# Optimization experiments

Measured on AMD Instinct MI355X. Metric: run time of the kernel, lower is better.

## Reference

```python
import jax, jax.numpy as jnp
import numpy as np

DIM = 192
HEADS = 6
B = 4
H = 64
W = 64
L = H * W  # kv length must equal h*w for the torch 'else' repeat branch
TOPK = 4
N_EXPERTS = 12
PADS = [0, 1, 2] * 4
GROUPS = [1] * 6 + [DIM] * 6


def conv2d(x, w, b=None, pad=0, groups=1):
    out = jax.lax.conv_general_dilated(
        x, w, (1, 1), [(pad, pad), (pad, pad)],
        dimension_numbers=("NCHW", "OIHW", "NCHW"),
        feature_group_count=groups)
    if b is not None:
        out = out + b[None, :, None, None]
    return out


def l2norm(x):
    # torch F.normalize(dim=-1): x / max(||x||_2, 1e-12)
    return x / jnp.maximum(jnp.linalg.norm(x, axis=-1, keepdims=True), 1e-12)


def attention_ca(I, T, proj_w):
    b, c, h, w = I.shape
    l = T.shape[2]
    # F.avg_pool1d(kv.transpose(1,2), 4) pools the CHANNEL dim, kernel=stride=4
    pooled = T.transpose(0, 2, 1).reshape(b, l, c // 4, 4).mean(-1)  # [b, l, c/4]
    x_pool = pooled.transpose(0, 2, 1)  # [b, c/4, l]
    q = l2norm(I.reshape(b, HEADS, c // HEADS, h * w))
    k = l2norm(x_pool.reshape(b, HEADS, c // (4 * HEADS), l))
    v = k  # v = normalize(x_pool) = k
    # h == 64 -> torch 'else' branch: repeat(1, 1, 4, 1) on channel dim
    k = jnp.tile(k, (1, 1, 4, 1))
    v = jnp.tile(v, (1, 1, 4, 1))
    attn = jax.nn.softmax(jnp.einsum("bhcl,bhdl->bhcd", q, k), axis=-1)
    out = jnp.einsum("bhcd,bhdl->bhcl", attn, v).reshape(b, c, h, w)
    return conv2d(out, proj_w)


def ex_forward(x, fmap, ex_ws, ex_bs, out_w, out_b):
    # AdaptiveAvgPool3d((1,1,12)) applied to a 4D tensor [b,c,h,w]:
    # full mean over dims 1 (c) and 2 (h), adaptive 12-bin pooling over dim 3 (w)
    m = fmap.mean(axis=(1, 2))  # [b, w]
    win = m.shape[-1]
    bins = [m[:, (i * win) // 12: -(-((i + 1) * win) // 12)].mean(-1) for i in range(12)]
    wvec = jax.nn.softmax(jnp.stack(bins, axis=-1), axis=-1)  # [b, 12]
    _, idx = jax.lax.top_k(wvec[0], TOPK)  # module uses batch element 0 only
    branches = [
        (lambda xx, j=j: conv2d(xx, ex_ws[j], ex_bs[j], pad=PADS[j], groups=GROUPS[j]))
        for j in range(N_EXPERTS)
    ]
    outs = [jax.lax.switch(idx[i], branches, x) for i in range(TOPK)]
    return conv2d(jnp.concatenate(outs, axis=1), out_w, out_b, pad=1)


def forward(I, T, temperature, ca1_proj_w, ex_ws, ex_bs, ex_out_w, ex_out_b,
            kv_w, kv_dw_w, q_dw_w, proj_w):
    b, c, h, w = I.shape
    fmap = attention_ca(I, T, ca1_proj_w)
    fmap = ex_forward(I, fmap, ex_ws, ex_bs, ex_out_w, ex_out_b)
    kv = conv2d(conv2d(fmap, kv_w), kv_dw_w, pad=1, groups=2 * c)
    k, v = jnp.split(kv, 2, axis=1)
    q = conv2d(fmap, q_dw_w, pad=1, groups=c)
    q = l2norm(q.reshape(b, HEADS, c // HEADS, h * w))
    k = l2norm(k.reshape(b, HEADS, c // HEADS, h * w))
    v = v.reshape(b, HEADS, c // HEADS, h * w)
    attn = jax.nn.softmax(jnp.einsum("bhcl,bhdl->bhcd", q, k) * temperature[None], axis=-1)
    out = jnp.einsum("bhcd,bhdl->bhcl", attn, v).reshape(b, c, h, w)
    return conv2d(out, proj_w)


def setup_inputs() -> dict:
    key = jax.random.key(0)
    ks = jax.random.split(key, 64)
    def rn(i, shape, s=0.05):
        return jax.random.normal(ks[i], shape, dtype=jnp.float32) * s
    d = DIM
    inp = {
        "I": rn(0, (B, d, H, W), 1.0),
        "T": rn(1, (B, d, L), 1.0),
        "temperature": jnp.ones((HEADS, 1, 1), dtype=jnp.float32),
        "ca1_proj_w": rn(2, (d, d, 1, 1)),
        "ex_out_w": rn(3, (d, 4 * d, 3, 3), 0.02),
        "ex_out_b": rn(4, (d,), 0.01),
        "kv_w": rn(5, (2 * d, d, 1, 1)),
        "kv_dw_w": rn(6, (2 * d, 1, 3, 3)),
        "q_dw_w": rn(7, (d, 1, 3, 3)),
        "proj_w": rn(8, (d, d, 1, 1)),
    }
    ksz = [1, 3, 5] * 4
    for j in range(N_EXPERTS):
        cin = d if j < 6 else 1
        inp[f"ex_w{j}"] = rn(10 + j, (d, cin, ksz[j], ksz[j]), 0.05)
        inp[f"ex_b{j}"] = rn(30 + j, (d,), 0.01)
    return inp


def reference(I, T, temperature, ca1_proj_w,
              ex_w0, ex_w1, ex_w2, ex_w3, ex_w4, ex_w5,
              ex_w6, ex_w7, ex_w8, ex_w9, ex_w10, ex_w11,
              ex_b0, ex_b1, ex_b2, ex_b3, ex_b4, ex_b5,
              ex_b6, ex_b7, ex_b8, ex_b9, ex_b10, ex_b11,
              ex_out_w, ex_out_b, kv_w, kv_dw_w, q_dw_w, proj_w):
    ex_ws = [ex_w0, ex_w1, ex_w2, ex_w3, ex_w4, ex_w5,
             ex_w6, ex_w7, ex_w8, ex_w9, ex_w10, ex_w11]
    ex_bs = [ex_b0, ex_b1, ex_b2, ex_b3, ex_b4, ex_b5,
             ex_b6, ex_b7, ex_b8, ex_b9, ex_b10, ex_b11]
    return forward(I, T, temperature, ca1_proj_w, ex_ws, ex_bs,
                   ex_out_w, ex_out_b, kv_w, kv_dw_w, q_dw_w, proj_w)
```

## Files before the change

kernel.cpp:

```cpp
#include <hip/hip_runtime.h>
#include <math.h>


struct ExPtrs { const float* w[12]; const float* b[12]; };
struct BfPtrs { const short* adt[6]; const float* bias[6]; };

typedef __attribute__((ext_vector_type(8))) short short8v;
typedef __attribute__((ext_vector_type(4))) short short4v;
typedef __attribute__((ext_vector_type(16))) float f32x16;

__device__ __forceinline__ void fma4(float4& a, float s, const float4& v) {
    a.x = fmaf(s, v.x, a.x); a.y = fmaf(s, v.y, a.y);
    a.z = fmaf(s, v.z, a.z); a.w = fmaf(s, v.w, a.w);
}

__device__ __forceinline__ short f2bf(float v) {
    unsigned u = __float_as_uint(v);
    return (short)((u + 0x7FFFu + ((u >> 16) & 1u)) >> 16);
}

__device__ __forceinline__ float bf2f(short v) {
    return __uint_as_float(((unsigned)(unsigned short)v) << 16);
}

__global__ void zero_kernel(float* __restrict__ p, int n) {
    for (int i = blockIdx.x * 256 + threadIdx.x; i < n; i += gridDim.x * 256) p[i] = 0.f;
}

__global__ void packIbf_kernel(const float* __restrict__ I, short* __restrict__ Ibf) {
    const int n = 4 * 68 * 68 * 192;
    for (int o = blockIdx.x * 256 + threadIdx.x; o < n; o += gridDim.x * 256) {
        int ch = o % 192;
        int t = o / 192;
        int xx = t % 68; t /= 68;
        int yy = t % 68;
        int b = t / 68;
        short v = 0;
        if (yy >= 2 && yy < 66 && xx >= 2 && xx < 66)
            v = f2bf(I[(((size_t)(b * 192 + ch)) << 12) + (yy - 2) * 64 + (xx - 2)]);
        Ibf[o] = v;
    }
}

__global__ void packAd_kernel(const float* __restrict__ w, short* __restrict__ Ad, int K2) {
    int n = K2 * 6 * 12 * 64 * 8;
    for (int o = blockIdx.x * 256 + threadIdx.x; o < n; o += gridDim.x * 256) {
        int j = o & 7;
        int t = o >> 3;
        int l = t & 63; t >>= 6;
        int ks = t % 12; t /= 12;
        int mt = t % 6;
        int tap = t / 6;
        int oc = mt * 32 + (l & 31);
        int ic = ks * 16 + (l >> 5) * 8 + j;
        Ad[o] = f2bf(w[(((size_t)oc * 192) + ic) * K2 + tap]);
    }
}

__global__ void packA_kernel(const float* __restrict__ exow, short* __restrict__ At) {
    const int n = 9 * 6 * 48 * 64 * 8;
    for (int o = blockIdx.x * 256 + threadIdx.x; o < n; o += gridDim.x * 256) {
        int j = o & 7;
        int t = o >> 3;
        int l = t & 63; t >>= 6;
        int ks = t % 48; t /= 48;
        int mt = t % 6;
        int tap = t / 6;
        int oc = mt * 32 + (l & 31);
        int icg = ks * 16 + (l >> 5) * 8 + j;
        At[o] = f2bf(exow[((size_t)oc * 768 + icg) * 9 + tap]);
    }
}

__global__ void wtr8_kernel(const float* __restrict__ w, float* __restrict__ wt,
                            int OCg, int IC, int K2) {
    int n = OCg * IC * K2 * 8;
    for (int o = blockIdx.x * 256 + threadIdx.x; o < n; o += gridDim.x * 256) {
        int u = o & 7;
        int t = o >> 3;
        int kk = t % K2;
        int t2 = t / K2;
        int ic = t2 % IC;
        int og = t2 / IC;
        wt[o] = w[(((size_t)(og * 8 + u)) * IC + ic) * K2 + kk];
    }
}

__global__ void packWdw_kernel(ExPtrs ep, float* __restrict__ wdwt) {
    int o = blockIdx.x * 256 + threadIdx.x;
    if (o >= 6 * 25 * 192) return;
    int ch = o % 192;
    int t = o / 192;
    int kk = t % 25;
    int e = t / 25;
    int j = e + 6;
    int K = 1 + 2 * (j % 3);
    int K2 = K * K;
    wdwt[o] = (kk < K2) ? ep.w[j][(size_t)ch * K2 + kk] : 0.f;
}


__global__ void pool64_kernel(const float* __restrict__ T, double* __restrict__ xp) {
    int j = blockIdx.x;
    for (int l = threadIdx.x; l < 4096; l += 256) {
        const float* t = T + ((size_t)(4 * j)) * 4096 + l;
        double s = (double)t[0] + (double)t[4096] + (double)t[2 * 4096] + (double)t[3 * 4096];
        xp[(size_t)j * 4096 + l] = 0.25 * s;
    }
}

__global__ void norm64_f32_kernel(const float* __restrict__ src, double* __restrict__ dst) {
    size_t off = (size_t)blockIdx.x * 4096;
    double acc = 0.0;
    for (int i = threadIdx.x; i < 4096; i += 256) { double v = src[off + i]; acc += v * v; }
    __shared__ double red[256];
    red[threadIdx.x] = acc; __syncthreads();
    for (int st = 128; st > 0; st >>= 1) {
        if (threadIdx.x < st) red[threadIdx.x] += red[threadIdx.x + st];
        __syncthreads();
    }
    double scale = 1.0 / fmax(sqrt(red[0]), 1e-12);
    for (int i = threadIdx.x; i < 4096; i += 256) dst[off + i] = src[off + i] * scale;
}

__global__ void norm64_f64_kernel(double* __restrict__ buf) {
    size_t off = (size_t)blockIdx.x * 4096;
    double acc = 0.0;
    for (int i = threadIdx.x; i < 4096; i += 256) { double v = buf[off + i]; acc += v * v; }
    __shared__ double red[256];
    red[threadIdx.x] = acc; __syncthreads();
    for (int st = 128; st > 0; st >>= 1) {
        if (threadIdx.x < st) red[threadIdx.x] += red[threadIdx.x + st];
        __syncthreads();
    }
    double scale = 1.0 / fmax(sqrt(red[0]), 1e-12);
    for (int i = threadIdx.x; i < 4096; i += 256) buf[off + i] *= scale;
}

__global__ void attnA64p_kernel(const double* __restrict__ qn, const double* __restrict__ kn,
                                double* __restrict__ PA) {
    int hh = blockIdx.x, cc = blockIdx.y;
    int t = threadIdx.x;
    int c = t >> 3, d = t & 7;
    const double* q = qn + ((size_t)(hh * 32 + c)) * 4096 + cc * 256;
    const double* k = kn + ((size_t)(hh * 8 + d)) * 4096 + cc * 256;
    double acc = 0.0;
    for (int i = 0; i < 256; ++i) acc += q[i] * k[i];
    PA[((size_t)((hh * 32 + c) * 8 + d)) * 16 + cc] = acc;
}

__global__ void attnA64r_kernel(const double* __restrict__ PA, double* __restrict__ A) {
    int hh = blockIdx.x;
    int t = threadIdx.x;
    int c = t >> 3, d = t & 7;
    double acc = 0.0;
    const double* p = PA + ((size_t)((hh * 32 + c) * 8 + d)) * 16;
    for (int cc = 0; cc < 16; ++cc) acc += p[cc];
    __shared__ double S[32][8];
    S[c][d] = acc;
    __syncthreads();
    if (t < 32) {
        double mx = -1e300;
        for (int j = 0; j < 8; ++j) mx = fmax(mx, S[t][j]);
        double e[8], sum = 0.0;
        for (int j = 0; j < 8; ++j) { e[j] = exp(S[t][j] - mx); sum += e[j]; }
        double inv = 1.0 / sum;
        for (int j = 0; j < 8; ++j) A[((size_t)(hh * 32 + t)) * 8 + j] = e[j] * inv;
    }
}

__global__ void kcol64_kernel(const double* __restrict__ kn, double* __restrict__ kcol) {
    int j = blockIdx.x, x = threadIdx.x;
    const double* s = kn + (size_t)j * 4096 + x;
    double acc = 0.0;
    for (int y = 0; y < 64; ++y) acc += s[y * 64];
    kcol[j * 64 + x] = acc;
}

__global__ void wsum64_kernel(const float* __restrict__ ca1, double* __restrict__ wsum) {
    int ic = threadIdx.x;
    if (ic >= 192) return;
    double acc = 0.0;
    for (int oc = 0; oc < 192; ++oc) acc += (double)ca1[(size_t)oc * 192 + ic];
    wsum[ic] = acc;
}

__global__ void mroute64_kernel(const double* __restrict__ A, const double* __restrict__ kcol,
                                const double* __restrict__ wsum, double* __restrict__ m) {
    int x = threadIdx.x;
    if (x >= 64) return;
    double acc = 0.0;
    for (int ic = 0; ic < 192; ++ic) {
        int hh = ic >> 5;
        double s = 0.0;
        #pragma unroll
        for (int d = 0; d < 8; ++d)
            s += A[(size_t)ic * 8 + d] * kcol[(hh * 8 + d) * 64 + x];
        acc += wsum[ic] * s;
    }
    m[x] = acc / (192.0 * 64.0);
}

__global__ void route64_kernel(const double* __restrict__ m, int* __restrict__ idx) {
    if (threadIdx.x != 0) return;
    double bins[12];
    for (int i = 0; i < 12; ++i) {
        int st = (i * 64) / 12;
        int en = ((i + 1) * 64 + 11) / 12;
        double s = 0.0;
        for (int j = st; j < en; ++j) s += m[j];
        bins[i] = s / (double)(en - st);
    }
    bool used[12] = {};
    for (int s = 0; s < 4; ++s) {
        int best = 0; double bv = -1e300;
        for (int j = 0; j < 12; ++j)
            if (!used[j] && bins[j] > bv) { best = j; bv = bins[j]; }
        used[best] = true;
        idx[s] = best;
    }
}


__global__ void rownorm_kernel(const float* __restrict__ src, float* __restrict__ dst) {
    size_t off = (size_t)blockIdx.x * 4096;
    const float* s = src + off;
    float acc = 0.f;
    for (int i = threadIdx.x; i < 4096; i += 256) { float v = s[i]; acc += v * v; }
    __shared__ float red[256];
    red[threadIdx.x] = acc; __syncthreads();
    for (int st = 128; st > 0; st >>= 1) {
        if (threadIdx.x < st) red[threadIdx.x] += red[threadIdx.x + st];
        __syncthreads();
    }
    float scale = 1.0f / fmaxf(sqrtf(red[0]), 1e-12f);
    float* d = dst + off;
    for (int i = threadIdx.x; i < 4096; i += 256) d[i] = s[i] * scale;
}

template<int KK>
__device__ __forceinline__ void dmf_body(const short* __restrict__ Ad,
                                         const short* __restrict__ Ibf,
                                         const float* __restrict__ bias,
                                         short* __restrict__ Ebf, int cslot,
                                         int b, int y, short* __restrict__ sb) {
    constexpr int P = (KK - 1) / 2;
    int tid = threadIdx.x;
    int lane = tid & 63, wave = tid >> 6;
    int u = blockIdx.y * 4 + wave;
    int mt = u >> 1, nt = u & 1;
    int c32 = lane & 31, hi = lane >> 5;
    f32x16 acc;
    #pragma unroll
    for (int r = 0; r < 16; ++r)
        acc[r] = bias[mt * 32 + (r & 3) + 8 * (r >> 2) + 4 * hi];
    for (int rr = 0; rr < KK; ++rr) {
        const short* src = Ibf + ((size_t)(b * 68 + y + 2 - P + rr)) * 68 * 192;
        if (rr > 0) __syncthreads();
        for (int g2 = tid; g2 < 68 * 24; g2 += 256) {
            int px = g2 / 24, ck = g2 % 24;
            *(short8v*)(sb + px * 200 + ck * 8) = *(const short8v*)(src + px * 192 + ck * 8);
        }
        __syncthreads();
        for (int dx = 0; dx < KK; ++dx) {
            int tap = rr * KK + dx;
            const short* Ab = Ad + (((size_t)(tap * 6 + mt)) * 12) * 512 + (size_t)lane * 8;
            const short* Bb = sb + ((2 - P) + dx + nt * 32 + c32) * 200 + hi * 8;
            #pragma unroll 4
            for (int ks = 0; ks < 12; ++ks) {
                short8v av = *(const short8v*)(Ab + ks * 512);
                short8v bv = *(const short8v*)(Bb + ks * 16);
                acc = __builtin_amdgcn_mfma_f32_32x32x16_bf16(av, bv, acc, 0, 0, 0);
            }
        }
    }
    int xo = nt * 32 + c32;
    short* dbase = Ebf + (((size_t)(b * 66 + y + 1)) * 68 + (xo + 1)) * 384
                   + cslot * 192 + mt * 32 + 4 * hi;
    #pragma unroll
    for (int g = 0; g < 4; ++g) {
        short4v o;
        #pragma unroll
        for (int r = 0; r < 4; ++r) o[r] = f2bf(acc[g * 4 + r]);
        *(short4v*)(dbase + g * 8) = o;
    }
}

__global__ void dense_mfma_kernel(BfPtrs bp, const short* __restrict__ Ibf,
                                  const int* __restrict__ idx, int slot,
                                  short* __restrict__ Ebf, int cslot) {
    __shared__ short sb[68 * 200];
    int j = idx[slot];
    j = j < 0 ? 0 : (j > 11 ? 11 : j);
    if (j >= 6) return;
    int y = blockIdx.x, b = blockIdx.z;
    int m = j % 3;
    if (m == 0) dmf_body<1>(bp.adt[j], Ibf, bp.bias[j], Ebf, cslot, b, y, sb);
    else if (m == 1) dmf_body<3>(bp.adt[j], Ibf, bp.bias[j], Ebf, cslot, b, y, sb);
    else dmf_body<5>(bp.adt[j], Ibf, bp.bias[j], Ebf, cslot, b, y, sb);
}

template<int KK>
__device__ __forceinline__ void dw_body(const short* __restrict__ Ibf,
                                        const float* __restrict__ wt,
                                        float bias,
                                        short* __restrict__ Ebf, int cslot,
                                        int b, int pg, int ch) {
    constexpr int P = (KK - 1) / 2;
    constexpr int K2 = KK * KK;
    float wreg[K2];
    #pragma unroll
    for (int kk = 0; kk < K2; ++kk) wreg[kk] = wt[kk * 192 + ch];
    #pragma unroll
    for (int u = 0; u < 4; ++u) {
        int px = pg * 4 + u;
        int y = px >> 6, x = px & 63;
        const short* base = Ibf + ((size_t)(b * 68 + y + 2 - P)) * 68 * 192
                            + (size_t)(x + 2 - P) * 192 + ch;
        float acc = bias;
        #pragma unroll
        for (int ky = 0; ky < KK; ++ky)
            #pragma unroll
            for (int kx = 0; kx < KK; ++kx)
                acc = fmaf(wreg[ky * KK + kx], bf2f(base[(ky * 68 + kx) * 192]), acc);
        Ebf[(((size_t)(b * 66 + y + 1)) * 68 + (x + 1)) * 384 + cslot * 192 + ch] = f2bf(acc);
    }
}

__global__ void dw_bf_kernel(const short* __restrict__ Ibf, const float* __restrict__ wdwt,
                             ExPtrs ep, const int* __restrict__ idx, int slot,
                             short* __restrict__ Ebf, int cslot) {
    int j = idx[slot];
    j = j < 0 ? 0 : (j > 11 ? 11 : j);
    if (j < 6) return;
    int ch = threadIdx.x;
    int pg = blockIdx.x, b = blockIdx.y;
    const float* wt = wdwt + (size_t)(j - 6) * 25 * 192;
    float bias = ep.b[j][ch];
    int m = j % 3;
    if (m == 0) dw_body<1>(Ibf, wt, bias, Ebf, cslot, b, pg, ch);
    else if (m == 1) dw_body<3>(Ibf, wt, bias, Ebf, cslot, b, pg, ch);
    else dw_body<5>(Ibf, wt, bias, Ebf, cslot, b, pg, ch);
}

__global__ void exout_mfma_kernel(const short* __restrict__ At, const short* __restrict__ Ebf,
                                  const float* __restrict__ bias, float* __restrict__ out,
                                  int pass) {
    __shared__ short sb[68 * 392];
    int y = blockIdx.x, b = blockIdx.z;
    int tid = threadIdx.x;
    int lane = tid & 63, wave = tid >> 6;
    int u = blockIdx.y * 4 + wave;
    int mt = u >> 1, nt = u & 1;
    int c32 = lane & 31, hi = lane >> 5;
    float* dst = out + ((size_t)(b * 192 + mt * 32)) * 4096 + y * 64 + nt * 32 + c32;
    f32x16 acc;
    if (pass == 0) {
        #pragma unroll
        for (int r = 0; r < 16; ++r)
            acc[r] = bias[mt * 32 + (r & 3) + 8 * (r >> 2) + 4 * hi];
    } else {
        #pragma unroll
        for (int r = 0; r < 16; ++r)
            acc[r] = dst[(size_t)((r & 3) + 8 * (r >> 2) + 4 * hi) * 4096];
    }
    for (int rr = 0; rr < 3; ++rr) {
        const short* src = Ebf + ((size_t)(b * 66 + y + rr)) * 68 * 384;
        if (rr > 0) __syncthreads();
        for (int g2 = tid; g2 < 68 * 48; g2 += 256) {
            int px = g2 / 48, ck = g2 % 48;
            *(short8v*)(sb + px * 392 + ck * 8) = *(const short8v*)(src + px * 384 + ck * 8);
        }
        __syncthreads();
        for (int dx = 0; dx < 3; ++dx) {
            int tap = rr * 3 + dx;
            const short* Ab = At + (((size_t)(tap * 6 + mt)) * 48 + pass * 24) * 512
                              + (size_t)lane * 8;
            const short* Bb = sb + (dx + nt * 32 + c32) * 392 + hi * 8;
            #pragma unroll 4
            for (int ks = 0; ks < 24; ++ks) {
                short8v av = *(const short8v*)(Ab + (size_t)ks * 512);
                short8v bv = *(const short8v*)(Bb + ks * 16);
                acc = __builtin_amdgcn_mfma_f32_32x32x16_bf16(av, bv, acc, 0, 0, 0);
            }
        }
    }
    #pragma unroll
    for (int r = 0; r < 16; ++r)
        dst[(size_t)((r & 3) + 8 * (r >> 2) + 4 * hi) * 4096] = acc[r];
}

__global__ void conv1x1_sw_kernel(const float* __restrict__ in, const float* __restrict__ wtg,
                                  float* __restrict__ out) {
    int tid = threadIdx.x;
    int xq = tid & 15, ry = tid >> 4;
    int tile = blockIdx.x, og = blockIdx.y, b = blockIdx.z;
    int p0 = tile * 1024 + ry * 64 + xq * 4;
    float4 acc[8] = {};
    const float* src = in + (size_t)b * 192 * 4096 + p0;
    const float* wp = wtg + (size_t)og * 192 * 8;
    for (int ic = 0; ic < 192; ic += 2) {
        float4 xv0 = *(const float4*)(src + (size_t)ic * 4096);
        float4 xv1 = *(const float4*)(src + (size_t)(ic + 1) * 4096);
        float4 wA0 = *(const float4*)(wp + ic * 8);
        float4 wB0 = *(const float4*)(wp + ic * 8 + 4);
        float4 wA1 = *(const float4*)(wp + ic * 8 + 8);
        float4 wB1 = *(const float4*)(wp + ic * 8 + 12);
        fma4(acc[0], wA0.x, xv0); fma4(acc[1], wA0.y, xv0);
        fma4(acc[2], wA0.z, xv0); fma4(acc[3], wA0.w, xv0);
        fma4(acc[4], wB0.x, xv0); fma4(acc[5], wB0.y, xv0);
        fma4(acc[6], wB0.z, xv0); fma4(acc[7], wB0.w, xv0);
        fma4(acc[0], wA1.x, xv1); fma4(acc[1], wA1.y, xv1);
        fma4(acc[2], wA1.z, xv1); fma4(acc[3], wA1.w, xv1);
        fma4(acc[4], wB1.x, xv1); fma4(acc[5], wB1.y, xv1);
        fma4(acc[6], wB1.z, xv1); fma4(acc[7], wB1.w, xv1);
    }
    float* dst = out + ((size_t)(b * 192 + og * 8)) * 4096 + p0;
    #pragma unroll
    for (int u = 0; u < 8; ++u)
        *(float4*)(dst + (size_t)u * 4096) = acc[u];
}

__global__ void dwconv_kernel(const float* __restrict__ in, const float* __restrict__ w,
                              float* __restrict__ out) {
    int l = blockIdx.x * 256 + threadIdx.x;
    int ch = blockIdx.y, b = blockIdx.z;
    int y = l >> 6, x = l & 63;
    const float* src = in + ((size_t)(b * 192 + ch)) * 4096;
    const float* wk = w + ch * 9;
    float acc = 0.f;
    #pragma unroll
    for (int ky = 0; ky < 3; ++ky)
        #pragma unroll
        for (int kx = 0; kx < 3; ++kx) {
            int yy = y + ky - 1, xx = x + kx - 1;
            if (yy >= 0 && yy < 64 && xx >= 0 && xx < 64)
                acc += wk[ky * 3 + kx] * src[yy * 64 + xx];
        }
    out[((size_t)(b * 192 + ch)) * 4096 + l] = acc;
}

__global__ void attnF_row_kernel(const float* __restrict__ qn, const float* __restrict__ kn,
                                 const float* __restrict__ temp, float* __restrict__ AF) {
    int row = blockIdx.x;
    int hh = (row >> 5) % 6, b = row / 192;
    int tid = threadIdx.x;
    const float* q = qn + ((size_t)(b * 192) + (row % 192)) * 4096;
    const float* kb = kn + ((size_t)(b * 192 + hh * 32)) * 4096;
    float acc[32];
    #pragma unroll
    for (int d = 0; d < 32; ++d) acc[d] = 0.f;
    for (int i = tid; i < 4096; i += 256) {
        float qv = q[i];
        #pragma unroll
        for (int d = 0; d < 32; ++d) acc[d] += qv * kb[(size_t)d * 4096 + i];
    }
    #pragma unroll
    for (int d = 0; d < 32; ++d) {
        acc[d] += __shfl_xor(acc[d], 32);
        acc[d] += __shfl_xor(acc[d], 16);
        acc[d] += __shfl_xor(acc[d], 8);
        acc[d] += __shfl_xor(acc[d], 4);
        acc[d] += __shfl_xor(acc[d], 2);
        acc[d] += __shfl_xor(acc[d], 1);
    }
    __shared__ float red[4][32];
    int wid = tid >> 6, lane = tid & 63;
    if (lane == 0) {
        #pragma unroll
        for (int d = 0; d < 32; ++d) red[wid][d] = acc[d];
    }
    __syncthreads();
    if (tid < 32) {
        float s = red[0][tid] + red[1][tid] + red[2][tid] + red[3][tid];
        s *= temp[hh];
        float mx = s;
        mx = fmaxf(mx, __shfl_xor(mx, 16));
        mx = fmaxf(mx, __shfl_xor(mx, 8));
        mx = fmaxf(mx, __shfl_xor(mx, 4));
        mx = fmaxf(mx, __shfl_xor(mx, 2));
        mx = fmaxf(mx, __shfl_xor(mx, 1));
        float e = expf(s - mx);
        float sum = e;
        sum += __shfl_xor(sum, 16);
        sum += __shfl_xor(sum, 8);
        sum += __shfl_xor(sum, 4);
        sum += __shfl_xor(sum, 2);
        sum += __shfl_xor(sum, 1);
        AF[(size_t)row * 32 + tid] = e / sum;
    }
}

__global__ void attnF_out_kernel(const float* __restrict__ AF, const float* __restrict__ v,
                                 float* __restrict__ out) {
    int l = blockIdx.x * 256 + threadIdx.x;
    int ch = blockIdx.y, b = blockIdx.z;
    int hh = ch >> 5, c = ch & 31;
    const float* a = AF + ((size_t)((b * 6 + hh) * 32 + c)) * 32;
    const float* vp = v + ((size_t)(b * 192 + hh * 32)) * 4096 + l;
    float acc = 0.f;
    #pragma unroll
    for (int d = 0; d < 32; ++d) acc += a[d] * vp[(size_t)d * 4096];
    out[((size_t)(b * 192 + ch)) * 4096 + l] = acc;
}

extern "C" void kernel_launch(void* const* d_in, const int* in_sizes, int n_in,
                              void* d_out, int out_size, void* d_ws, size_t ws_size,
                              hipStream_t stream) {
    const float* I    = (const float*)d_in[0];
    const float* T    = (const float*)d_in[1];
    const float* temp = (const float*)d_in[2];
    const float* ca1  = (const float*)d_in[3];
    const float* exow = (const float*)d_in[4];
    const float* exob = (const float*)d_in[5];
    const float* kvw  = (const float*)d_in[6];
    const float* kvdw = (const float*)d_in[7];
    const float* qdw  = (const float*)d_in[8];
    const float* projw= (const float*)d_in[9];
    ExPtrs ep;
    for (int j = 0; j < 12; ++j) {
        ep.w[j] = (const float*)d_in[10 + 2 * j];
        ep.b[j] = (const float*)d_in[11 + 2 * j];
    }

    float* ws   = (float*)d_ws;
    float* AF   = ws;
    int*   idxb = (int*)(ws + 24576);
    float* R0   = ws + 32768;
    float* R1   = R0 + 3145728;
    float* IbfF = R1 + 3145728;
    float* EbfF = IbfF + 3551232;
    double* dsm = (double*)(EbfF + 3446784);
    double* A64 = dsm;
    double* m64 = dsm + 1536;
    double* PA  = dsm + 1600;
    double* kcol = dsm + 26176;
    double* wsum = dsm + 29248;
    float* wtkv   = (float*)(dsm + 29440);
    float* wtproj = wtkv + 73728;
    float* wdwt   = wtproj + 36864;
    short* At     = (short*)(wdwt + 28800);
    short* Adt    = At + 1327104;
    size_t adtoff[6] = {0, 36864, 368640, 1290240, 1327104, 1658880};
    double* xpool64 = (double*)R0;
    double* qn64    = (double*)(R0 + 393216);
    short* Ibf = (short*)IbfF;
    short* Ebf = (short*)EbfF;
    float* KN = IbfF;
    float* V  = EbfF;
    BfPtrs bp;
    for (int j = 0; j < 6; ++j) { bp.adt[j] = Adt + adtoff[j]; bp.bias[j] = ep.b[j]; }
    float* out  = (float*)d_out;

    dim3 g(16, 192, 4), gs8(4, 24, 4), gmf(64, 3, 4), gdw(1024, 4);

    for (int j = 0; j < 6; ++j) {
        int KK = 1 + 2 * (j % 3);
        packAd_kernel<<<512, 256, 0, stream>>>(ep.w[j], Adt + adtoff[j], KK * KK);
    }
    packA_kernel<<<1024, 256, 0, stream>>>(exow, At);
    wtr8_kernel<<<256, 256, 0, stream>>>(kvw, wtkv, 48, 192, 1);
    wtr8_kernel<<<256, 256, 0, stream>>>(projw, wtproj, 24, 192, 1);
    packWdw_kernel<<<113, 256, 0, stream>>>(ep, wdwt);
    packIbf_kernel<<<2048, 256, 0, stream>>>(I, Ibf);

    pool64_kernel<<<48, 256, 0, stream>>>(T, xpool64);
    norm64_f32_kernel<<<192, 256, 0, stream>>>(I, qn64);
    norm64_f64_kernel<<<48, 256, 0, stream>>>(xpool64);
    attnA64p_kernel<<<dim3(6, 16), 256, 0, stream>>>(qn64, xpool64, PA);
    attnA64r_kernel<<<6, 256, 0, stream>>>(PA, A64);
    kcol64_kernel<<<48, 64, 0, stream>>>(xpool64, kcol);
    wsum64_kernel<<<1, 192, 0, stream>>>(ca1, wsum);
    mroute64_kernel<<<1, 64, 0, stream>>>(A64, kcol, wsum, m64);
    route64_kernel<<<1, 64, 0, stream>>>(m64, idxb);

    zero_kernel<<<2048, 256, 0, stream>>>(EbfF, 3446784);
    for (int s = 0; s < 4; ++s) {
        dense_mfma_kernel<<<gmf, 256, 0, stream>>>(bp, Ibf, idxb, s, Ebf, s & 1);
        dw_bf_kernel<<<gdw, 192, 0, stream>>>(Ibf, wdwt, ep, idxb, s, Ebf, s & 1);
        if (s == 1)
            exout_mfma_kernel<<<gmf, 256, 0, stream>>>(At, Ebf, exob, R1, 0);
        if (s == 3)
            exout_mfma_kernel<<<gmf, 256, 0, stream>>>(At, Ebf, exob, R1, 1);
    }

    conv1x1_sw_kernel<<<gs8, 256, 0, stream>>>(R1, wtkv, R0);
    dwconv_kernel<<<g, 256, 0, stream>>>(R0, kvdw, KN);
    rownorm_kernel<<<768, 256, 0, stream>>>(KN, KN);
    dwconv_kernel<<<g, 256, 0, stream>>>(R1, qdw, R0);
    rownorm_kernel<<<768, 256, 0, stream>>>(R0, R0);
    attnF_row_kernel<<<768, 256, 0, stream>>>(R0, KN, temp, AF);
    conv1x1_sw_kernel<<<gs8, 256, 0, stream>>>(R1, wtkv + 36864, R0);
    dwconv_kernel<<<g, 256, 0, stream>>>(R0, kvdw + 192 * 9, V);

    attnF_out_kernel<<<g, 256, 0, stream>>>(AF, V, R0);
    conv1x1_sw_kernel<<<gs8, 256, 0, stream>>>(R0, wtproj, out);
}
```

Baseline: 573.6 us.

## Give each MFMA wave both column tiles and split K into even/odd accumulators

In the dense expert conv and the output 3x3 conv MFMA kernels, each wave now computes one 32-row M tile across both 32-wide N tiles. Each A fragment is therefore loaded once and reused for two MFMAs. The K loop is split into even and odd accumulator chains that are summed at the end, which breaks the serial MFMA dependency. Blocks shrink to 3 waves (192 threads) and the grid y drops to 2. This raises register use (four 16-float accumulators per wave) and lowers the wave count per block, which may cut occupancy.

```diff
diff --git a/kernel.cpp b/kernel.cpp
--- a/kernel.cpp
+++ b/kernel.cpp
@@ -247,17 +247,18 @@
     constexpr int P = (KK - 1) / 2;
     int tid = threadIdx.x;
     int lane = tid & 63, wave = tid >> 6;
-    int u = blockIdx.y * 4 + wave;
-    int mt = u >> 1, nt = u & 1;
+    int mt = blockIdx.y * 3 + wave;
     int c32 = lane & 31, hi = lane >> 5;
-    f32x16 acc;
-    #pragma unroll
-    for (int r = 0; r < 16; ++r)
-        acc[r] = bias[mt * 32 + (r & 3) + 8 * (r >> 2) + 4 * hi];
+    f32x16 a0e, a0o, a1e, a1o;
+    #pragma unroll
+    for (int r = 0; r < 16; ++r) {
+        float bv_ = bias[mt * 32 + (r & 3) + 8 * (r >> 2) + 4 * hi];
+        a0e[r] = bv_; a1e[r] = bv_; a0o[r] = 0.f; a1o[r] = 0.f;
+    }
     for (int rr = 0; rr < KK; ++rr) {
         const short* src = Ibf + ((size_t)(b * 68 + y + 2 - P + rr)) * 68 * 192;
         if (rr > 0) __syncthreads();
-        for (int g2 = tid; g2 < 68 * 24; g2 += 256) {
+        for (int g2 = tid; g2 < 68 * 24; g2 += 192) {
             int px = g2 / 24, ck = g2 % 24;
             *(short8v*)(sb + px * 200 + ck * 8) = *(const short8v*)(src + px * 192 + ck * 8);
         }
@@ -265,24 +266,37 @@
         for (int dx = 0; dx < KK; ++dx) {
             int tap = rr * KK + dx;
             const short* Ab = Ad + (((size_t)(tap * 6 + mt)) * 12) * 512 + (size_t)lane * 8;
-            const short* Bb = sb + ((2 - P) + dx + nt * 32 + c32) * 200 + hi * 8;
-            #pragma unroll 4
-            for (int ks = 0; ks < 12; ++ks) {
-                short8v av = *(const short8v*)(Ab + ks * 512);
-                short8v bv = *(const short8v*)(Bb + ks * 16);
-                acc = __builtin_amdgcn_mfma_f32_32x32x16_bf16(av, bv, acc, 0, 0, 0);
+            const short* Bb0 = sb + ((2 - P) + dx + c32) * 200 + hi * 8;
+            const short* Bb1 = Bb0 + 32 * 200;
+            #pragma unroll 2
+            for (int k2 = 0; k2 < 6; ++k2) {
+                short8v ave = *(const short8v*)(Ab + (2 * k2) * 512);
+                short8v avo = *(const short8v*)(Ab + (2 * k2 + 1) * 512);
+                short8v b0e = *(const short8v*)(Bb0 + (2 * k2) * 16);
+                short8v b0o = *(const short8v*)(Bb0 + (2 * k2 + 1) * 16);
+                short8v b1e = *(const short8v*)(Bb1 + (2 * k2) * 16);
+                short8v b1o = *(const short8v*)(Bb1 + (2 * k2 + 1) * 16);
+                a0e = __builtin_amdgcn_mfma_f32_32x32x16_bf16(ave, b0e, a0e, 0, 0, 0);
+                a1e = __builtin_amdgcn_mfma_f32_32x32x16_bf16(ave, b1e, a1e, 0, 0, 0);
+                a0o = __builtin_amdgcn_mfma_f32_32x32x16_bf16(avo, b0o, a0o, 0, 0, 0);
+                a1o = __builtin_amdgcn_mfma_f32_32x32x16_bf16(avo, b1o, a1o, 0, 0, 0);
             }
         }
     }
-    int xo = nt * 32 + c32;
-    short* dbase = Ebf + (((size_t)(b * 66 + y + 1)) * 68 + (xo + 1)) * 384
-                   + cslot * 192 + mt * 32 + 4 * hi;
+    short* db0 = Ebf + (((size_t)(b * 66 + y + 1)) * 68 + (c32 + 1)) * 384
+                 + cslot * 192 + mt * 32 + 4 * hi;
+    short* db1 = Ebf + (((size_t)(b * 66 + y + 1)) * 68 + (32 + c32 + 1)) * 384
+                 + cslot * 192 + mt * 32 + 4 * hi;
     #pragma unroll
     for (int g = 0; g < 4; ++g) {
-        short4v o;
-        #pragma unroll
-        for (int r = 0; r < 4; ++r) o[r] = f2bf(acc[g * 4 + r]);
-        *(short4v*)(dbase + g * 8) = o;
+        short4v o0, o1;
+        #pragma unroll
+        for (int r = 0; r < 4; ++r) {
+            o0[r] = f2bf(a0e[g * 4 + r] + a0o[g * 4 + r]);
+            o1[r] = f2bf(a1e[g * 4 + r] + a1o[g * 4 + r]);
+        }
+        *(short4v*)(db0 + g * 8) = o0;
+        *(short4v*)(db1 + g * 8) = o1;
     }
 }
 
@@ -350,24 +364,29 @@
     int y = blockIdx.x, b = blockIdx.z;
     int tid = threadIdx.x;
     int lane = tid & 63, wave = tid >> 6;
-    int u = blockIdx.y * 4 + wave;
-    int mt = u >> 1, nt = u & 1;
+    int mt = blockIdx.y * 3 + wave;
     int c32 = lane & 31, hi = lane >> 5;
-    float* dst = out + ((size_t)(b * 192 + mt * 32)) * 4096 + y * 64 + nt * 32 + c32;
-    f32x16 acc;
+    float* d0 = out + ((size_t)(b * 192 + mt * 32)) * 4096 + y * 64 + c32;
+    float* d1 = d0 + 32;
+    f32x16 a0e, a0o, a1e, a1o;
     if (pass == 0) {
         #pragma unroll
-        for (int r = 0; r < 16; ++r)
-            acc[r] = bias[mt * 32 + (r & 3) + 8 * (r >> 2) + 4 * hi];
+        for (int r = 0; r < 16; ++r) {
+            float bv_ = bias[mt * 32 + (r & 3) + 8 * (r >> 2) + 4 * hi];
+            a0e[r] = bv_; a1e[r] = bv_; a0o[r] = 0.f; a1o[r] = 0.f;
+        }
     } else {
         #pragma unroll
-        for (int r = 0; r < 16; ++r)
-            acc[r] = dst[(size_t)((r & 3) + 8 * (r >> 2) + 4 * hi) * 4096];
+        for (int r = 0; r < 16; ++r) {
+            size_t ro = (size_t)((r & 3) + 8 * (r >> 2) + 4 * hi) * 4096;
+            a0e[r] = d0[ro]; a1e[r] = d1[ro];
+            a0o[r] = 0.f; a1o[r] = 0.f;
+        }
     }
     for (int rr = 0; rr < 3; ++rr) {
         const short* src = Ebf + ((size_t)(b * 66 + y + rr)) * 68 * 384;
         if (rr > 0) __syncthreads();
-        for (int g2 = tid; g2 < 68 * 48; g2 += 256) {
+        for (int g2 = tid; g2 < 68 * 48; g2 += 192) {
             int px = g2 / 48, ck = g2 % 48;
             *(short8v*)(sb + px * 392 + ck * 8) = *(const short8v*)(src + px * 384 + ck * 8);
         }
@@ -376,18 +395,29 @@
             int tap = rr * 3 + dx;
             const short* Ab = At + (((size_t)(tap * 6 + mt)) * 48 + pass * 24) * 512
                               + (size_t)lane * 8;
-            const short* Bb = sb + (dx + nt * 32 + c32) * 392 + hi * 8;
-            #pragma unroll 4
-            for (int ks = 0; ks < 24; ++ks) {
-                short8v av = *(const short8v*)(Ab + (size_t)ks * 512);
-                short8v bv = *(const short8v*)(Bb + ks * 16);
-                acc = __builtin_amdgcn_mfma_f32_32x32x16_bf16(av, bv, acc, 0, 0, 0);
+            const short* Bb0 = sb + (dx + c32) * 392 + hi * 8;
+            const short* Bb1 = Bb0 + 32 * 392;
+            #pragma unroll 2
+            for (int k2 = 0; k2 < 12; ++k2) {
+                short8v ave = *(const short8v*)(Ab + (size_t)(2 * k2) * 512);
+                short8v avo = *(const short8v*)(Ab + (size_t)(2 * k2 + 1) * 512);
+                short8v b0e = *(const short8v*)(Bb0 + (2 * k2) * 16);
+                short8v b0o = *(const short8v*)(Bb0 + (2 * k2 + 1) * 16);
+                short8v b1e = *(const short8v*)(Bb1 + (2 * k2) * 16);
+                short8v b1o = *(const short8v*)(Bb1 + (2 * k2 + 1) * 16);
+                a0e = __builtin_amdgcn_mfma_f32_32x32x16_bf16(ave, b0e, a0e, 0, 0, 0);
+                a1e = __builtin_amdgcn_mfma_f32_32x32x16_bf16(ave, b1e, a1e, 0, 0, 0);
+                a0o = __builtin_amdgcn_mfma_f32_32x32x16_bf16(avo, b0o, a0o, 0, 0, 0);
+                a1o = __builtin_amdgcn_mfma_f32_32x32x16_bf16(avo, b1o, a1o, 0, 0, 0);
             }
         }
     }
     #pragma unroll
-    for (int r = 0; r < 16; ++r)
-        dst[(size_t)((r & 3) + 8 * (r >> 2) + 4 * hi) * 4096] = acc[r];
+    for (int r = 0; r < 16; ++r) {
+        size_t ro = (size_t)((r & 3) + 8 * (r >> 2) + 4 * hi) * 4096;
+        d0[ro] = a0e[r] + a0o[r];
+        d1[ro] = a1e[r] + a1o[r];
+    }
 }
 
 __global__ void conv1x1_sw_kernel(const float* __restrict__ in, const float* __restrict__ wtg,
@@ -552,7 +582,7 @@
     for (int j = 0; j < 6; ++j) { bp.adt[j] = Adt + adtoff[j]; bp.bias[j] = ep.b[j]; }
     float* out  = (float*)d_out;
 
-    dim3 g(16, 192, 4), gs8(4, 24, 4), gmf(64, 3, 4), gdw(1024, 4);
+    dim3 g(16, 192, 4), gs8(4, 24, 4), gmf(64, 2, 4), gdw(1024, 4);
 
     for (int j = 0; j < 6; ++j) {
         int KK = 1 + 2 * (j % 3);
@@ -576,12 +606,12 @@
 
     zero_kernel<<<2048, 256, 0, stream>>>(EbfF, 3446784);
     for (int s = 0; s < 4; ++s) {
-        dense_mfma_kernel<<<gmf, 256, 0, stream>>>(bp, Ibf, idxb, s, Ebf, s & 1);
+        dense_mfma_kernel<<<gmf, 192, 0, stream>>>(bp, Ibf, idxb, s, Ebf, s & 1);
         dw_bf_kernel<<<gdw, 192, 0, stream>>>(Ibf, wdwt, ep, idxb, s, Ebf, s & 1);
         if (s == 1)
-            exout_mfma_kernel<<<gmf, 256, 0, stream>>>(At, Ebf, exob, R1, 0);
+            exout_mfma_kernel<<<gmf, 192, 0, stream>>>(At, Ebf, exob, R1, 0);
         if (s == 3)
-            exout_mfma_kernel<<<gmf, 256, 0, stream>>>(At, Ebf, exob, R1, 1);
+            exout_mfma_kernel<<<gmf, 192, 0, stream>>>(At, Ebf, exob, R1, 1);
     }
 
     conv1x1_sw_kernel<<<gs8, 256, 0, stream>>>(R1, wtkv, R0);
```

Measured after the change: 622.6 us. 1.09x slower.
